# Performance work log

Measured on AMD Instinct MI355X. Metric: run time of the kernel, lower is better.

Reference implementation:

```python
import jax, jax.numpy as jnp
import numpy as np

B, S, D, E, K = 4, 4096, 1024, 8, 2


def setup_inputs() -> dict:
    key = jax.random.key(0)
    k0, k1, k2 = jax.random.split(key, 3)
    return {
        "x": jax.random.normal(k0, (B, S, D), dtype=jnp.float32),
        "gate_w": jax.random.normal(k1, (E, D), dtype=jnp.float32) * 0.02,   # torch Linear weight [out,in]
        "gate_b": jnp.zeros((E,), dtype=jnp.float32),
        "expert_w": jax.random.normal(k2, (E, D, D), dtype=jnp.float32) * 0.02,  # [E, out, in]
        "expert_b": jnp.zeros((E, D), dtype=jnp.float32),
    }


def reference(x, gate_w, gate_b, expert_w, expert_b):
    b, s, d = x.shape
    h = x.reshape(-1, d)                                   # [T, D], T = b*s
    # Router: gate linear -> softmax (float32) -> top-k -> renormalize
    router_logits = h @ gate_w.T + gate_b                  # [T, E]
    probs = jax.nn.softmax(router_logits.astype(jnp.float32), axis=-1)
    router_weights, selected_experts = jax.lax.top_k(probs, K)  # [T, K]
    router_weights = router_weights / router_weights.sum(axis=-1, keepdims=True)
    router_weights = router_weights.astype(h.dtype)
    # Combine weights per (token, expert): sum of top-k weights routed to each expert
    cw = (jax.nn.one_hot(selected_experts, E, dtype=h.dtype)
          * router_weights[..., None]).sum(axis=1)         # [T, E]
    # Dense-equivalent of gather-linear-scatter: every expert on every token,
    # then weighted combine (mathematically identical to the per-expert loop).
    expert_out = jnp.einsum('td,eod->teo', h, expert_w) + expert_b[None]  # [T, E, D]
    out = jnp.einsum('te,teo->to', cw, expert_out)         # [T, D]
    return out.reshape(b, s, d), router_logits, selected_experts
```

## Files before the change

### kernel.cpp

```cpp
#include <hip/hip_runtime.h>
#include <hip/hip_bf16.h>

#define T_TOK 16384
#define D_DIM 1024
#define E_EXP 8
#define NPAIR 28

#define BM 128
#define BN 128
#define BK 64
#define NT_K (D_DIM / BK)

#define CNT_STRIDE 64

typedef __attribute__((ext_vector_type(4))) float f32x4;
typedef __attribute__((ext_vector_type(2))) float f32x2;
typedef __attribute__((ext_vector_type(8))) short bf16x8;
typedef __attribute__((ext_vector_type(4))) unsigned short u16x4;

static __device__ __forceinline__ unsigned short f2bf(float f) {
    unsigned int u = __float_as_uint(f);
    unsigned int r = 0x7FFFu + ((u >> 16) & 1u);
    return (unsigned short)((u + r) >> 16);
}

#define GLOAD_LDS16(gp, lp) \
    __builtin_amdgcn_global_load_lds( \
        (const __attribute__((address_space(1))) void*)(gp), \
        (__attribute__((address_space(3))) void*)(lp), 16, 0, 0)

__global__ __launch_bounds__(256) void convert_w_kernel(
    const float* __restrict__ w, unsigned short* __restrict__ o) {
    const int n4 = (E_EXP * D_DIM * D_DIM) / 4;
    for (int i = blockIdx.x * 256 + threadIdx.x; i < n4; i += gridDim.x * 256) {
        f32x4 v = ((const f32x4*)w)[i];
        u16x4 p;
        p[0] = f2bf(v[0]); p[1] = f2bf(v[1]); p[2] = f2bf(v[2]); p[3] = f2bf(v[3]);
        ((u16x4*)o)[i] = p;
    }
}

#define TPB_TOK 64
__global__ __launch_bounds__(256) void router_kernel(
    const float* __restrict__ x, const float* __restrict__ gate_w,
    const float* __restrict__ gate_b, float* __restrict__ out_logits,
    float* __restrict__ out_sel, int* __restrict__ counts,
    int* __restrict__ pair_token, f32x2* __restrict__ pair_w,
    unsigned short* __restrict__ xbf) {
    __shared__ float gw[E_EXP][D_DIM];
    __shared__ float gb_s[E_EXP];
    __shared__ float logits_s[TPB_TOK][E_EXP];
    __shared__ int   cnt_local[NPAIR];
    __shared__ int   gbase[NPAIR];
    __shared__ int   ent_p[TPB_TOK];
    __shared__ int   ent_pos[TPB_TOK];
    __shared__ f32x2 ent_w[TPB_TOK];

    const int tid = threadIdx.x;
    for (int i = tid; i < E_EXP * D_DIM; i += 256) gw[0][i] = gate_w[i];
    if (tid < E_EXP) gb_s[tid] = gate_b[tid];
    if (tid < NPAIR) cnt_local[tid] = 0;
    __syncthreads();

    const int lane = tid & 63, wv = tid >> 6;
    const int tl = lane >> 2, g = lane & 3;
    const int jt = wv * 16 + tl;
    const int t = blockIdx.x * TPB_TOK + jt;

    float acc[E_EXP] = {};
    const f32x4* xr = (const f32x4*)(x + (size_t)t * D_DIM);
    u16x4* xw = (u16x4*)(xbf + (size_t)t * D_DIM);
    for (int i = g; i < D_DIM / 4; i += 4) {
        f32x4 xv = xr[i];
        u16x4 pk;
        pk[0] = f2bf(xv[0]); pk[1] = f2bf(xv[1]); pk[2] = f2bf(xv[2]); pk[3] = f2bf(xv[3]);
        xw[i] = pk;
        #pragma unroll
        for (int e = 0; e < E_EXP; ++e) {
            f32x4 gv = ((const f32x4*)(&gw[e][0]))[i];
            acc[e] += xv[0] * gv[0] + xv[1] * gv[1] + xv[2] * gv[2] + xv[3] * gv[3];
        }
    }
    #pragma unroll
    for (int e = 0; e < E_EXP; ++e) {
        float v = acc[e];
        v += __shfl_xor(v, 1, 64);
        v += __shfl_xor(v, 2, 64);
        acc[e] = v;
    }
    if (g == 0) {
        float l[E_EXP], p[E_EXP];
        float m = -1e30f;
        #pragma unroll
        for (int e = 0; e < E_EXP; ++e) { l[e] = acc[e] + gb_s[e]; m = fmaxf(m, l[e]); }
        float s = 0.f;
        #pragma unroll
        for (int e = 0; e < E_EXP; ++e) { p[e] = expf(l[e] - m); s += p[e]; }
        #pragma unroll
        for (int e = 0; e < E_EXP; ++e) p[e] /= s;
        int e0 = 0; float p0 = p[0];
        #pragma unroll
        for (int e = 1; e < E_EXP; ++e) if (p[e] > p0) { p0 = p[e]; e0 = e; }
        int e1 = -1; float p1 = -1e30f;
        #pragma unroll
        for (int e = 0; e < E_EXP; ++e) if (e != e0 && p[e] > p1) { p1 = p[e]; e1 = e; }
        float denom = p0 + p1;
        float w0 = p0 / denom, w1 = p1 / denom;
        #pragma unroll
        for (int e = 0; e < E_EXP; ++e) logits_s[jt][e] = l[e];
        out_sel[t * 2 + 0] = (float)e0;
        out_sel[t * 2 + 1] = (float)e1;
        int lo = min(e0, e1), hi = max(e0, e1);
        float wl = (e0 < e1) ? w0 : w1;
        float wh = (e0 < e1) ? w1 : w0;
        int pp = (lo * (15 - lo)) / 2 + (hi - lo - 1);
        int pos = atomicAdd(&cnt_local[pp], 1);
        ent_p[jt] = pp; ent_pos[jt] = pos;
        f32x2 wv2; wv2[0] = wl; wv2[1] = wh;
        ent_w[jt] = wv2;
    }
    __syncthreads();
    if (tid < NPAIR) gbase[tid] = atomicAdd(&counts[tid * CNT_STRIDE], cnt_local[tid]);
    if (tid < TPB_TOK * E_EXP / 4) {
        f32x4 v = ((const f32x4*)&logits_s[0][0])[tid];
        ((f32x4*)(out_logits + (size_t)blockIdx.x * TPB_TOK * E_EXP))[tid] = v;
    }
    __syncthreads();
    if (g == 0) {
        int pp = ent_p[jt];
        int pos = gbase[pp] + ent_pos[jt];
        pair_token[pp * T_TOK + pos] = t;
        pair_w[pp * T_TOK + pos] = ent_w[jt];
    }
}

__global__ void schedule_kernel(const int* __restrict__ counts,
                                int* __restrict__ tiles, int* __restrict__ ntiles) {
    if (threadIdx.x != 0 || blockIdx.x != 0) return;
    int idx = 0, p = 0;
    for (int lo = 0; lo < E_EXP - 1; ++lo)
        for (int hi = lo + 1; hi < E_EXP; ++hi, ++p) {
            int c = counts[p * CNT_STRIDE];
            for (int m = 0; m < c; m += BM)
                tiles[idx++] = p | (lo << 5) | (hi << 8) | (m << 12);
        }
    *ntiles = idx;
}

__global__ __launch_bounds__(256, 2) void moe_gemm_kernel(
    const unsigned short* __restrict__ xbf, const unsigned short* __restrict__ wbf,
    const float* __restrict__ expert_b, const int* __restrict__ counts,
    const int* __restrict__ ntiles, const int* __restrict__ tiles,
    const int* __restrict__ pair_token, const f32x2* __restrict__ pair_w,
    float* __restrict__ out) {
    const int flat = blockIdx.x;
    const int cls = flat & 7;
    const int nt  = (flat >> 3) & 7;
    const int sup = flat >> 6;
    const int gidx = sup * 8 + cls;
    if (gidx >= *ntiles) return;
    const int entry = tiles[gidx];
    const int p = entry & 31;
    const int lo = (entry >> 5) & 7, hi = (entry >> 8) & 7;
    const int m_base = entry >> 12;
    const int cnt = counts[p * CNT_STRIDE];
    const int n_base = nt * BN;

    __shared__ unsigned short As[BM * BK];
    __shared__ unsigned short B0s[BM * BK];
    __shared__ unsigned short B1s[BM * BK];
    __shared__ int tok_s[BM];
    __shared__ f32x2 w_s[BM];

    const int tid = threadIdx.x;
    if (tid < BM) {
        int m = m_base + tid;
        int mc = (m < cnt) ? m : (cnt - 1);
        tok_s[tid] = pair_token[p * T_TOK + mc];
        w_s[tid]   = pair_w[p * T_TOK + mc];
    }
    __syncthreads();

    const int lane = tid & 63;
    const int w = tid >> 6;
    const int lr = lane & 15, lk = lane >> 4;
    const int wr = w >> 1, wc = w & 1;

    const int srow = lane >> 3;
    const int scol = 8 * ((lane & 7) ^ srow);
    const unsigned short* wb0 = wbf + ((size_t)lo << 20);
    const unsigned short* wb1 = wbf + ((size_t)hi << 20);
    const unsigned short* agp[4];
    const unsigned short* b0gp[4];
    const unsigned short* b1gp[4];
    int loff[4];
    #pragma unroll
    for (int i = 0; i < 4; ++i) {
        int R = i * 32 + w * 8 + srow;
        agp[i]  = xbf + (size_t)tok_s[R] * D_DIM + scol;
        b0gp[i] = wb0 + (size_t)(n_base + R) * D_DIM + scol;
        b1gp[i] = wb1 + (size_t)(n_base + R) * D_DIM + scol;
        loff[i] = (i * 32 + w * 8) * BK;
    }

    f32x4 acc0[4][4] = {};
    f32x4 acc1[4][4] = {};

    for (int k0 = 0; k0 < D_DIM; k0 += BK) {
        #pragma unroll
        for (int i = 0; i < 4; ++i) {
            GLOAD_LDS16(agp[i] + k0, &As[loff[i]]);
            GLOAD_LDS16(b0gp[i] + k0, &B0s[loff[i]]);
            GLOAD_LDS16(b1gp[i] + k0, &B1s[loff[i]]);
        }
        __syncthreads();
        #pragma unroll
        for (int kk = 0; kk < 2; ++kk) {
            bf16x8 a[4], b[4], c[4];
            #pragma unroll
            for (int m = 0; m < 4; ++m) {
                int R = wr * 64 + m * 16 + lr;
                int cb = (kk * 64 + lk * 16) ^ ((R & 7) << 4);
                a[m] = *(const bf16x8*)((const char*)As + R * 128 + cb);
            }
            #pragma unroll
            for (int n = 0; n < 4; ++n) {
                int R = wc * 64 + n * 16 + lr;
                int cb = (kk * 64 + lk * 16) ^ ((R & 7) << 4);
                b[n] = *(const bf16x8*)((const char*)B0s + R * 128 + cb);
            }
            #pragma unroll
            for (int m = 0; m < 4; ++m)
                #pragma unroll
                for (int n = 0; n < 4; ++n)
                    acc0[m][n] = __builtin_amdgcn_mfma_f32_16x16x32_bf16(a[m], b[n], acc0[m][n], 0, 0, 0);
            #pragma unroll
            for (int n = 0; n < 4; ++n) {
                int R = wc * 64 + n * 16 + lr;
                int cb = (kk * 64 + lk * 16) ^ ((R & 7) << 4);
                c[n] = *(const bf16x8*)((const char*)B1s + R * 128 + cb);
            }
            #pragma unroll
            for (int m = 0; m < 4; ++m)
                #pragma unroll
                for (int n = 0; n < 4; ++n)
                    acc1[m][n] = __builtin_amdgcn_mfma_f32_16x16x32_bf16(a[m], c[n], acc1[m][n], 0, 0, 0);
        }
        __syncthreads();
    }

    float blo[4], bhi[4];
    #pragma unroll
    for (int n = 0; n < 4; ++n) {
        int gn = n_base + wc * 64 + n * 16 + lr;
        blo[n] = expert_b[lo * D_DIM + gn];
        bhi[n] = expert_b[hi * D_DIM + gn];
    }
    #pragma unroll
    for (int m = 0; m < 4; ++m) {
        #pragma unroll
        for (int j = 0; j < 4; ++j) {
            int mi = wr * 64 + m * 16 + lk * 4 + j;
            if (m_base + mi >= cnt) continue;
            int tk = tok_s[mi];
            f32x2 wgt = w_s[mi];
            size_t obase = (size_t)tk * D_DIM + n_base + wc * 64 + lr;
            #pragma unroll
            for (int n = 0; n < 4; ++n)
                out[obase + n * 16] = wgt[0] * (acc0[m][n][j] + blo[n])
                                    + wgt[1] * (acc1[m][n][j] + bhi[n]);
        }
    }
}

extern "C" void kernel_launch(void* const* d_in, const int* in_sizes, int n_in,
                              void* d_out, int out_size, void* d_ws, size_t ws_size,
                              hipStream_t stream) {
    const float* x        = (const float*)d_in[0];
    const float* gate_w   = (const float*)d_in[1];
    const float* gate_b   = (const float*)d_in[2];
    const float* expert_w = (const float*)d_in[3];
    const float* expert_b = (const float*)d_in[4];

    float* out        = (float*)d_out;
    float* out_logits = out + (size_t)T_TOK * D_DIM;
    float* out_sel    = out_logits + (size_t)T_TOK * E_EXP;

    char* ws = (char*)d_ws;
    unsigned short* wbf = (unsigned short*)ws;
    unsigned short* xbf = (unsigned short*)(ws + 16777216);
    size_t off = 50331648;
    int*   counts     = (int*)(ws + off);
    int*   ntiles     = (int*)(ws + off + 8192);
    int*   tiles      = (int*)(ws + off + 8192 + 256);
    int*   pair_token = (int*)(ws + off + 16384);
    f32x2* pair_w     = (f32x2*)(ws + off + 16384 + 1835008);

    hipMemsetAsync(counts, 0, NPAIR * CNT_STRIDE * sizeof(int), stream);

    convert_w_kernel<<<2048, 256, 0, stream>>>(expert_w, wbf);
    router_kernel<<<T_TOK / TPB_TOK, 256, 0, stream>>>(x, gate_w, gate_b, out_logits,
                                                       out_sel, counts, pair_token,
                                                       pair_w, xbf);
    schedule_kernel<<<1, 64, 0, stream>>>(counts, tiles, ntiles);
    moe_gemm_kernel<<<20 * 64, 256, 0, stream>>>(xbf, wbf, expert_b, counts,
                                                 ntiles, tiles, pair_token, pair_w, out);
}
```

Baseline: 148.1 us.

## Triple-buffer LDS K-loop with async global-to-LDS prefetch and MFMA priority

Replaces the single-buffered BK=64 main loop with a three-stage ring of BK=32 LDS slots. Global-to-LDS loads are issued two stages ahead and gated by explicit vmcnt waits and raw barriers, so memory latency overlaps MFMA work. The LDS swizzle is changed to suit the 64-byte rows, and s_setprio is raised around the MFMA bursts. The cost is more barriers per unit of K work and tighter reliance on hand-counted waitcnts; LDS use stays about the same (3x32 versus 64 columns).

```diff
diff --git a/kernel.cpp b/kernel.cpp
--- a/kernel.cpp
+++ b/kernel.cpp
@@ -8,8 +8,9 @@
 
 #define BM 128
 #define BN 128
-#define BK 64
-#define NT_K (D_DIM / BK)
+#define BK3 32
+#define NT3 (D_DIM / BK3)
+#define SLOT (BM * BK3)
 
 #define CNT_STRIDE 64
 
@@ -166,9 +167,9 @@
     const int cnt = counts[p * CNT_STRIDE];
     const int n_base = nt * BN;
 
-    __shared__ unsigned short As[BM * BK];
-    __shared__ unsigned short B0s[BM * BK];
-    __shared__ unsigned short B1s[BM * BK];
+    __shared__ unsigned short As[3][SLOT];
+    __shared__ unsigned short B0s[3][SLOT];
+    __shared__ unsigned short B1s[3][SLOT];
     __shared__ int tok_s[BM];
     __shared__ f32x2 w_s[BM];
 
@@ -185,69 +186,76 @@
     const int w = tid >> 6;
     const int lr = lane & 15, lk = lane >> 4;
     const int wr = w >> 1, wc = w & 1;
-
-    const int srow = lane >> 3;
-    const int scol = 8 * ((lane & 7) ^ srow);
+    const int jsw = (lk ^ ((lr >> 1) & 3)) * 8;
+
+    const int srow = tid >> 2;
+    const int scol = 8 * ((tid & 3) ^ ((srow >> 1) & 3));
     const unsigned short* wb0 = wbf + ((size_t)lo << 20);
     const unsigned short* wb1 = wbf + ((size_t)hi << 20);
-    const unsigned short* agp[4];
-    const unsigned short* b0gp[4];
-    const unsigned short* b1gp[4];
-    int loff[4];
-    #pragma unroll
-    for (int i = 0; i < 4; ++i) {
-        int R = i * 32 + w * 8 + srow;
-        agp[i]  = xbf + (size_t)tok_s[R] * D_DIM + scol;
-        b0gp[i] = wb0 + (size_t)(n_base + R) * D_DIM + scol;
-        b1gp[i] = wb1 + (size_t)(n_base + R) * D_DIM + scol;
-        loff[i] = (i * 32 + w * 8) * BK;
-    }
+    const unsigned short* agp0  = xbf + (size_t)tok_s[srow] * D_DIM + scol;
+    const unsigned short* agp1  = xbf + (size_t)tok_s[64 + srow] * D_DIM + scol;
+    const unsigned short* b0gp0 = wb0 + (size_t)(n_base + srow) * D_DIM + scol;
+    const unsigned short* b0gp1 = wb0 + (size_t)(n_base + 64 + srow) * D_DIM + scol;
+    const unsigned short* b1gp0 = wb1 + (size_t)(n_base + srow) * D_DIM + scol;
+    const unsigned short* b1gp1 = wb1 + (size_t)(n_base + 64 + srow) * D_DIM + scol;
+    const int l0 = w * 512;
+    const int l1 = 2048 + w * 512;
 
     f32x4 acc0[4][4] = {};
     f32x4 acc1[4][4] = {};
 
-    for (int k0 = 0; k0 < D_DIM; k0 += BK) {
-        #pragma unroll
-        for (int i = 0; i < 4; ++i) {
-            GLOAD_LDS16(agp[i] + k0, &As[loff[i]]);
-            GLOAD_LDS16(b0gp[i] + k0, &B0s[loff[i]]);
-            GLOAD_LDS16(b1gp[i] + k0, &B1s[loff[i]]);
-        }
-        __syncthreads();
-        #pragma unroll
-        for (int kk = 0; kk < 2; ++kk) {
-            bf16x8 a[4], b[4], c[4];
-            #pragma unroll
-            for (int m = 0; m < 4; ++m) {
-                int R = wr * 64 + m * 16 + lr;
-                int cb = (kk * 64 + lk * 16) ^ ((R & 7) << 4);
-                a[m] = *(const bf16x8*)((const char*)As + R * 128 + cb);
-            }
-            #pragma unroll
-            for (int n = 0; n < 4; ++n) {
-                int R = wc * 64 + n * 16 + lr;
-                int cb = (kk * 64 + lk * 16) ^ ((R & 7) << 4);
-                b[n] = *(const bf16x8*)((const char*)B0s + R * 128 + cb);
-            }
-            #pragma unroll
-            for (int m = 0; m < 4; ++m)
-                #pragma unroll
-                for (int n = 0; n < 4; ++n)
-                    acc0[m][n] = __builtin_amdgcn_mfma_f32_16x16x32_bf16(a[m], b[n], acc0[m][n], 0, 0, 0);
-            #pragma unroll
-            for (int n = 0; n < 4; ++n) {
-                int R = wc * 64 + n * 16 + lr;
-                int cb = (kk * 64 + lk * 16) ^ ((R & 7) << 4);
-                c[n] = *(const bf16x8*)((const char*)B1s + R * 128 + cb);
-            }
-            #pragma unroll
-            for (int m = 0; m < 4; ++m)
-                #pragma unroll
-                for (int n = 0; n < 4; ++n)
-                    acc1[m][n] = __builtin_amdgcn_mfma_f32_16x16x32_bf16(a[m], c[n], acc1[m][n], 0, 0, 0);
-        }
-        __syncthreads();
-    }
+#define STAGE_ADV(s) do { \
+        GLOAD_LDS16(agp0,  &As[s][l0]);  GLOAD_LDS16(agp1,  &As[s][l1]); \
+        GLOAD_LDS16(b0gp0, &B0s[s][l0]); GLOAD_LDS16(b0gp1, &B0s[s][l1]); \
+        GLOAD_LDS16(b1gp0, &B1s[s][l0]); GLOAD_LDS16(b1gp1, &B1s[s][l1]); \
+        agp0 += BK3; agp1 += BK3; b0gp0 += BK3; b0gp1 += BK3; b1gp0 += BK3; b1gp1 += BK3; \
+    } while (0)
+
+#define STEP(s, sn, ISSUE, VMC) do { \
+        if (ISSUE) STAGE_ADV(sn); \
+        asm volatile("s_waitcnt vmcnt(" #VMC ")" ::: "memory"); \
+        __builtin_amdgcn_s_barrier(); \
+        bf16x8 a[4], b[4]; \
+        _Pragma("unroll") \
+        for (int m = 0; m < 4; ++m) \
+            a[m] = *(const bf16x8*)&As[s][(wr * 64 + m * 16 + lr) * BK3 + jsw]; \
+        _Pragma("unroll") \
+        for (int n = 0; n < 4; ++n) \
+            b[n] = *(const bf16x8*)&B0s[s][(wc * 64 + n * 16 + lr) * BK3 + jsw]; \
+        __builtin_amdgcn_s_setprio(1); \
+        _Pragma("unroll") \
+        for (int m = 0; m < 4; ++m) \
+            _Pragma("unroll") \
+            for (int n = 0; n < 4; ++n) \
+                acc0[m][n] = __builtin_amdgcn_mfma_f32_16x16x32_bf16(a[m], b[n], acc0[m][n], 0, 0, 0); \
+        __builtin_amdgcn_s_setprio(0); \
+        _Pragma("unroll") \
+        for (int n = 0; n < 4; ++n) \
+            b[n] = *(const bf16x8*)&B1s[s][(wc * 64 + n * 16 + lr) * BK3 + jsw]; \
+        __builtin_amdgcn_s_setprio(1); \
+        _Pragma("unroll") \
+        for (int m = 0; m < 4; ++m) \
+            _Pragma("unroll") \
+            for (int n = 0; n < 4; ++n) \
+                acc1[m][n] = __builtin_amdgcn_mfma_f32_16x16x32_bf16(a[m], b[n], acc1[m][n], 0, 0, 0); \
+        __builtin_amdgcn_s_setprio(0); \
+        asm volatile("s_waitcnt lgkmcnt(0)" ::: "memory"); \
+        __builtin_amdgcn_s_barrier(); \
+    } while (0)
+
+    STAGE_ADV(0);
+    STAGE_ADV(1);
+
+    #pragma unroll 1
+    for (int grp = 0; grp < 10; ++grp) {
+        STEP(0, 2, 1, 12);
+        STEP(1, 0, 1, 12);
+        STEP(2, 1, 1, 12);
+    }
+    STEP(0, 0, 0, 6);
+    STEP(1, 0, 0, 0);
+#undef STEP
+#undef STAGE_ADV
 
     float blo[4], bhi[4];
     #pragma unroll
```

Result: slower. 159.4 us (+7.6%).

## Fold tile scheduling into GEMM prologue and restructure router for coalesced rows

Applied to the files above, without the earlier changes.

Removes the single-thread schedule_kernel launch. Each GEMM block now finds its (pair, m-tile) by running a wave-level prefix scan over the per-pair counts. The router moves to 512 threads, with one wave per token row reading fully coalesced 256-float chunks and reducing across the wave. A second pass then does softmax and top-k per token. This drops one kernel launch and a serial scheduling step, at the cost of redundant scan work in every GEMM block and an extra barrier in the router.

```diff
diff --git a/kernel.cpp b/kernel.cpp
--- a/kernel.cpp
+++ b/kernel.cpp
@@ -9,7 +9,6 @@
 #define BM 128
 #define BN 128
 #define BK 64
-#define NT_K (D_DIM / BK)
 
 #define CNT_STRIDE 64
 
@@ -40,8 +39,8 @@
     }
 }
 
-#define TPB_TOK 64
-__global__ __launch_bounds__(256) void router_kernel(
+#define RTOK 64
+__global__ __launch_bounds__(512) void router_kernel(
     const float* __restrict__ x, const float* __restrict__ gate_w,
     const float* __restrict__ gate_b, float* __restrict__ out_logits,
     float* __restrict__ out_sel, int* __restrict__ counts,
@@ -49,50 +48,58 @@
     unsigned short* __restrict__ xbf) {
     __shared__ float gw[E_EXP][D_DIM];
     __shared__ float gb_s[E_EXP];
-    __shared__ float logits_s[TPB_TOK][E_EXP];
+    __shared__ float logits_s[RTOK][E_EXP];
     __shared__ int   cnt_local[NPAIR];
     __shared__ int   gbase[NPAIR];
-    __shared__ int   ent_p[TPB_TOK];
-    __shared__ int   ent_pos[TPB_TOK];
-    __shared__ f32x2 ent_w[TPB_TOK];
+    __shared__ int   ent_p[RTOK];
+    __shared__ int   ent_pos[RTOK];
+    __shared__ f32x2 ent_w[RTOK];
 
     const int tid = threadIdx.x;
-    for (int i = tid; i < E_EXP * D_DIM; i += 256) gw[0][i] = gate_w[i];
+    for (int i = tid; i < E_EXP * D_DIM; i += 512) gw[0][i] = gate_w[i];
     if (tid < E_EXP) gb_s[tid] = gate_b[tid];
     if (tid < NPAIR) cnt_local[tid] = 0;
     __syncthreads();
 
     const int lane = tid & 63, wv = tid >> 6;
-    const int tl = lane >> 2, g = lane & 3;
-    const int jt = wv * 16 + tl;
-    const int t = blockIdx.x * TPB_TOK + jt;
-
-    float acc[E_EXP] = {};
-    const f32x4* xr = (const f32x4*)(x + (size_t)t * D_DIM);
-    u16x4* xw = (u16x4*)(xbf + (size_t)t * D_DIM);
-    for (int i = g; i < D_DIM / 4; i += 4) {
-        f32x4 xv = xr[i];
-        u16x4 pk;
-        pk[0] = f2bf(xv[0]); pk[1] = f2bf(xv[1]); pk[2] = f2bf(xv[2]); pk[3] = f2bf(xv[3]);
-        xw[i] = pk;
+    for (int j = 0; j < RTOK / 8; ++j) {
+        const int jt = wv * (RTOK / 8) + j;
+        const int t = blockIdx.x * RTOK + jt;
+        const float* xrow = x + (size_t)t * D_DIM;
+        unsigned short* xbrow = xbf + (size_t)t * D_DIM;
+        float acc[E_EXP] = {};
+        #pragma unroll
+        for (int c = 0; c < 4; ++c) {
+            const int col = c * 256 + lane * 4;
+            f32x4 xv = *(const f32x4*)(xrow + col);
+            u16x4 pk;
+            pk[0] = f2bf(xv[0]); pk[1] = f2bf(xv[1]); pk[2] = f2bf(xv[2]); pk[3] = f2bf(xv[3]);
+            *(u16x4*)(xbrow + col) = pk;
+            #pragma unroll
+            for (int e = 0; e < E_EXP; ++e) {
+                f32x4 gv = *(const f32x4*)(&gw[e][col]);
+                acc[e] += xv[0] * gv[0] + xv[1] * gv[1] + xv[2] * gv[2] + xv[3] * gv[3];
+            }
+        }
         #pragma unroll
         for (int e = 0; e < E_EXP; ++e) {
-            f32x4 gv = ((const f32x4*)(&gw[e][0]))[i];
-            acc[e] += xv[0] * gv[0] + xv[1] * gv[1] + xv[2] * gv[2] + xv[3] * gv[3];
-        }
-    }
-    #pragma unroll
-    for (int e = 0; e < E_EXP; ++e) {
-        float v = acc[e];
-        v += __shfl_xor(v, 1, 64);
-        v += __shfl_xor(v, 2, 64);
-        acc[e] = v;
-    }
-    if (g == 0) {
+            float v = acc[e];
+            #pragma unroll
+            for (int off = 32; off > 0; off >>= 1) v += __shfl_xor(v, off, 64);
+            acc[e] = v;
+        }
+        if (lane == 0) {
+            #pragma unroll
+            for (int e = 0; e < E_EXP; ++e) logits_s[jt][e] = acc[e] + gb_s[e];
+        }
+    }
+    __syncthreads();
+    if (tid < RTOK) {
+        const int t = blockIdx.x * RTOK + tid;
         float l[E_EXP], p[E_EXP];
         float m = -1e30f;
         #pragma unroll
-        for (int e = 0; e < E_EXP; ++e) { l[e] = acc[e] + gb_s[e]; m = fmaxf(m, l[e]); }
+        for (int e = 0; e < E_EXP; ++e) { l[e] = logits_s[tid][e]; m = fmaxf(m, l[e]); }
         float s = 0.f;
         #pragma unroll
         for (int e = 0; e < E_EXP; ++e) { p[e] = expf(l[e] - m); s += p[e]; }
@@ -106,8 +113,6 @@
         for (int e = 0; e < E_EXP; ++e) if (e != e0 && p[e] > p1) { p1 = p[e]; e1 = e; }
         float denom = p0 + p1;
         float w0 = p0 / denom, w1 = p1 / denom;
-        #pragma unroll
-        for (int e = 0; e < E_EXP; ++e) logits_s[jt][e] = l[e];
         out_sel[t * 2 + 0] = (float)e0;
         out_sel[t * 2 + 1] = (float)e1;
         int lo = min(e0, e1), hi = max(e0, e1);
@@ -115,42 +120,28 @@
         float wh = (e0 < e1) ? w1 : w0;
         int pp = (lo * (15 - lo)) / 2 + (hi - lo - 1);
         int pos = atomicAdd(&cnt_local[pp], 1);
-        ent_p[jt] = pp; ent_pos[jt] = pos;
+        ent_p[tid] = pp; ent_pos[tid] = pos;
         f32x2 wv2; wv2[0] = wl; wv2[1] = wh;
-        ent_w[jt] = wv2;
+        ent_w[tid] = wv2;
     }
     __syncthreads();
     if (tid < NPAIR) gbase[tid] = atomicAdd(&counts[tid * CNT_STRIDE], cnt_local[tid]);
-    if (tid < TPB_TOK * E_EXP / 4) {
+    if (tid < RTOK * E_EXP / 4) {
         f32x4 v = ((const f32x4*)&logits_s[0][0])[tid];
-        ((f32x4*)(out_logits + (size_t)blockIdx.x * TPB_TOK * E_EXP))[tid] = v;
-    }
-    __syncthreads();
-    if (g == 0) {
-        int pp = ent_p[jt];
-        int pos = gbase[pp] + ent_pos[jt];
-        pair_token[pp * T_TOK + pos] = t;
-        pair_w[pp * T_TOK + pos] = ent_w[jt];
-    }
-}
-
-__global__ void schedule_kernel(const int* __restrict__ counts,
-                                int* __restrict__ tiles, int* __restrict__ ntiles) {
-    if (threadIdx.x != 0 || blockIdx.x != 0) return;
-    int idx = 0, p = 0;
-    for (int lo = 0; lo < E_EXP - 1; ++lo)
-        for (int hi = lo + 1; hi < E_EXP; ++hi, ++p) {
-            int c = counts[p * CNT_STRIDE];
-            for (int m = 0; m < c; m += BM)
-                tiles[idx++] = p | (lo << 5) | (hi << 8) | (m << 12);
-        }
-    *ntiles = idx;
+        ((f32x4*)(out_logits + (size_t)blockIdx.x * RTOK * E_EXP))[tid] = v;
+    }
+    __syncthreads();
+    if (tid < RTOK) {
+        int pp = ent_p[tid];
+        int pos = gbase[pp] + ent_pos[tid];
+        pair_token[pp * T_TOK + pos] = blockIdx.x * RTOK + tid;
+        pair_w[pp * T_TOK + pos] = ent_w[tid];
+    }
 }
 
 __global__ __launch_bounds__(256, 2) void moe_gemm_kernel(
     const unsigned short* __restrict__ xbf, const unsigned short* __restrict__ wbf,
     const float* __restrict__ expert_b, const int* __restrict__ counts,
-    const int* __restrict__ ntiles, const int* __restrict__ tiles,
     const int* __restrict__ pair_token, const f32x2* __restrict__ pair_w,
     float* __restrict__ out) {
     const int flat = blockIdx.x;
@@ -158,12 +149,41 @@
     const int nt  = (flat >> 3) & 7;
     const int sup = flat >> 6;
     const int gidx = sup * 8 + cls;
-    if (gidx >= *ntiles) return;
-    const int entry = tiles[gidx];
-    const int p = entry & 31;
-    const int lo = (entry >> 5) & 7, hi = (entry >> 8) & 7;
-    const int m_base = entry >> 12;
-    const int cnt = counts[p * CNT_STRIDE];
+
+    __shared__ int hdr[5];
+    const int tid = threadIdx.x;
+    if (tid < 64) {
+        int c = (tid < NPAIR) ? counts[tid * CNT_STRIDE] : 0;
+        int ntp = (c + BM - 1) >> 7;
+        int s = ntp;
+        #pragma unroll
+        for (int off = 1; off < 64; off <<= 1) {
+            int v = __shfl_up(s, off, 64);
+            if (tid >= off) s += v;
+        }
+        int excl = s - ntp;
+        bool mine = (tid < NPAIR) && (gidx >= excl) && (gidx < s);
+        unsigned long long mb = __ballot(mine);
+        int p = mb ? (__ffsll((long long)mb) - 1) : 0;
+        int exclp = __shfl(excl, p, 64);
+        int cp = __shfl(c, p, 64);
+        if (tid == 0) {
+            if (mb == 0) { hdr[0] = -1; }
+            else {
+                int lo = 0, q = p;
+                while (q >= 7 - lo) { q -= 7 - lo; ++lo; }
+                hdr[0] = lo; hdr[1] = lo + 1 + q;
+                hdr[2] = (gidx - exclp) * BM; hdr[3] = cp; hdr[4] = p;
+            }
+        }
+    }
+    __syncthreads();
+    const int lo = hdr[0];
+    if (lo < 0) return;
+    const int hi = hdr[1];
+    const int m_base = hdr[2];
+    const int cnt = hdr[3];
+    const int p = hdr[4];
     const int n_base = nt * BN;
 
     __shared__ unsigned short As[BM * BK];
@@ -172,7 +192,6 @@
     __shared__ int tok_s[BM];
     __shared__ f32x2 w_s[BM];
 
-    const int tid = threadIdx.x;
     if (tid < BM) {
         int m = m_base + tid;
         int mc = (m < cnt) ? m : (cnt - 1);
@@ -291,18 +310,15 @@
     unsigned short* xbf = (unsigned short*)(ws + 16777216);
     size_t off = 50331648;
     int*   counts     = (int*)(ws + off);
-    int*   ntiles     = (int*)(ws + off + 8192);
-    int*   tiles      = (int*)(ws + off + 8192 + 256);
     int*   pair_token = (int*)(ws + off + 16384);
     f32x2* pair_w     = (f32x2*)(ws + off + 16384 + 1835008);
 
     hipMemsetAsync(counts, 0, NPAIR * CNT_STRIDE * sizeof(int), stream);
 
     convert_w_kernel<<<2048, 256, 0, stream>>>(expert_w, wbf);
-    router_kernel<<<T_TOK / TPB_TOK, 256, 0, stream>>>(x, gate_w, gate_b, out_logits,
-                                                       out_sel, counts, pair_token,
-                                                       pair_w, xbf);
-    schedule_kernel<<<1, 64, 0, stream>>>(counts, tiles, ntiles);
+    router_kernel<<<T_TOK / RTOK, 512, 0, stream>>>(x, gate_w, gate_b, out_logits,
+                                                    out_sel, counts, pair_token,
+                                                    pair_w, xbf);
     moe_gemm_kernel<<<20 * 64, 256, 0, stream>>>(xbf, wbf, expert_b, counts,
-                                                 ntiles, tiles, pair_token, pair_w, out);
-}
+                                                 pair_token, pair_w, out);
+}
```

Measured after the change: 134.7 us. -9.1%, faster.
